# Performance work log

Hardware: AMD Instinct MI355X
Metric: run time of the kernel (lower is better)

Reference implementation:

```python
import jax, jax.numpy as jnp
import numpy as np

D, NH, T = 1024, 16, 2048
DH = D // NH
SCALE = 1.0 / np.sqrt(DH)


def setup_inputs() -> dict:
    key = jax.random.key(0)
    k1, k2, k3, k4 = jax.random.split(key, 4)
    x = jax.random.normal(k1, (4, T, D), dtype=jnp.float32)
    # torch nn.Linear weights: y = x @ W.T ; init scaled like default
    qkv_w = jax.random.normal(k2, (3 * D, D), dtype=jnp.float32) * (1.0 / np.sqrt(D))
    o_w = jax.random.normal(k3, (D, D), dtype=jnp.float32) * (1.0 / np.sqrt(D))
    o_b = jax.random.normal(k4, (D,), dtype=jnp.float32) * 0.01
    return {"x": x, "qkv_w": qkv_w, "o_w": o_w, "o_b": o_b}


def reference(x, qkv_w, o_w, o_b):
    b, t, c = x.shape
    qkv = jnp.einsum('btc,fc->btf', x, qkv_w)  # [b,t,3d]
    q, k, v = jnp.split(qkv, 3, axis=-1)
    # [b, nh, t, dh]
    q = q.reshape(b, t, NH, DH).transpose(0, 2, 1, 3)
    k = k.reshape(b, t, NH, DH).transpose(0, 2, 1, 3)
    v = v.reshape(b, t, NH, DH).transpose(0, 2, 1, 3)
    w = jnp.einsum('bhqd,bhkd->bhqk', q, k) * SCALE
    causal = jnp.tril(jnp.ones((t, t), dtype=bool))
    w = jnp.where(causal[None, None], w, -jnp.inf)
    w = jax.nn.softmax(w, axis=-1)
    out = jnp.einsum('bhqk,bhkd->bhqd', w, v)
    out = out.transpose(0, 2, 1, 3).reshape(b, t, c)
    return jnp.einsum('btc,oc->bto', out, o_w) + o_b
```

## Files before the change

### kernel.cpp

```cpp
#include <hip/hip_runtime.h>
#include <stdint.h>

#define TSEQ   2048
#define SCALE_ATTN 0.125f

typedef __attribute__((ext_vector_type(8))) short bf16x8;
typedef __attribute__((ext_vector_type(4))) short short4v;
typedef __attribute__((ext_vector_type(4))) float f32x4;

__device__ __forceinline__ short f2bf(float f) {
  unsigned u = __float_as_uint(f);
  u = (u + 0x7fffu + ((u >> 16) & 1u)) >> 16;
  return (short)u;
}

__device__ __forceinline__ void async16(const void* gsrc, void* ldst) {
  __builtin_amdgcn_global_load_lds((__attribute__((address_space(1))) void*)(void*)gsrc,
                                   (__attribute__((address_space(3))) void*)ldst, 16, 0, 0);
}

__global__ void cast_f32_bf16(const float* __restrict__ src, short* __restrict__ dst, int n) {
  int i = (blockIdx.x * blockDim.x + threadIdx.x) * 4;
  if (i >= n) return;
  float4 v = *(const float4*)(src + i);
  short4v o;
  o[0] = f2bf(v.x); o[1] = f2bf(v.y); o[2] = f2bf(v.z); o[3] = f2bf(v.w);
  *(short4v*)(dst + i) = o;
}

template<int MODE>
__global__ __launch_bounds__(256, 2) void gemm_bt(
    const short* __restrict__ A, const short* __restrict__ B,
    void* __restrict__ C, short* __restrict__ Cvt, const float* __restrict__ bias,
    int M, int N, int K)
{
  __shared__ char ldsA[128 * 128];
  __shared__ char ldsB[128 * 128];

  const int tid  = threadIdx.x;
  const int lane = tid & 63;
  const int w    = tid >> 6;
  const int wrow = w >> 1, wcol = w & 1;
  const int l15  = lane & 15;
  const int klo  = (lane >> 4) << 4;

  int nwg = gridDim.x, orig = blockIdx.x;
  int qq = nwg >> 3, rr = nwg & 7;
  int xcd = orig & 7, lid = orig >> 3;
  int wgid = (xcd < rr ? xcd * (qq + 1) : rr * (qq + 1) + (xcd - rr) * qq) + lid;
  const int nbx = N >> 7;
  const int by = wgid / nbx, bx = wgid - by * nbx;
  const int m0 = by << 7, n0 = bx << 7;

  const char* Abase = (const char*)A + (size_t)m0 * K * 2;
  const char* Bbase = (const char*)B + (size_t)n0 * K * 2;
  const int rowstride = K * 2;

  const int srow  = tid >> 3;
  const int scolb = (tid & 7) << 4;

  f32x4 acc[4][4] = {};

  const int nk = K >> 6;
  for (int kk = 0; kk < nk; ++kk) {
    if (kk) __syncthreads();
    const int kbyte = kk << 7;
    #pragma unroll
    for (int p = 0; p < 4; ++p) {
      int row = p * 32 + srow;
      int sc  = scolb ^ ((row & 7) << 4);
      async16(Abase + (size_t)row * rowstride + kbyte + sc, ldsA + row * 128 + scolb);
      async16(Bbase + (size_t)row * rowstride + kbyte + sc, ldsB + row * 128 + scolb);
    }
    __syncthreads();

    bf16x8 af[2][4], bf[2][4];
    #pragma unroll
    for (int ks = 0; ks < 2; ++ks)
      #pragma unroll
      for (int mi = 0; mi < 4; ++mi) {
        int row = wrow * 64 + mi * 16 + l15;
        af[ks][mi] = *(const bf16x8*)(ldsA + row * 128 + ((ks * 64 + klo) ^ ((row & 7) << 4)));
      }
    #pragma unroll
    for (int ks = 0; ks < 2; ++ks)
      #pragma unroll
      for (int ni = 0; ni < 4; ++ni) {
        int row = wcol * 64 + ni * 16 + l15;
        bf[ks][ni] = *(const bf16x8*)(ldsB + row * 128 + ((ks * 64 + klo) ^ ((row & 7) << 4)));
      }
    #pragma unroll
    for (int mi = 0; mi < 4; ++mi)
      #pragma unroll
      for (int ni = 0; ni < 4; ++ni) {
        acc[mi][ni] = __builtin_amdgcn_mfma_f32_16x16x32_bf16(af[0][mi], bf[0][ni], acc[mi][ni], 0, 0, 0);
        acc[mi][ni] = __builtin_amdgcn_mfma_f32_16x16x32_bf16(af[1][mi], bf[1][ni], acc[mi][ni], 0, 0, 0);
      }
  }

  const int rbase = (lane >> 4) << 2;
  #pragma unroll
  for (int mi = 0; mi < 4; ++mi)
    #pragma unroll
    for (int ni = 0; ni < 4; ++ni) {
      const int col  = n0 + wcol * 64 + ni * 16 + l15;
      const int row0 = m0 + wrow * 64 + mi * 16 + rbase;
      if (MODE == 0) {
        #pragma unroll
        for (int j = 0; j < 4; ++j)
          ((float*)C)[(size_t)(row0 + j) * N + col] = acc[mi][ni][j] + bias[col];
      } else {
        if (n0 < 2048) {
          #pragma unroll
          for (int j = 0; j < 4; ++j)
            ((short*)C)[(size_t)(row0 + j) * 2048 + col] = f2bf(acc[mi][ni][j]);
        } else {
          short4v o;
          #pragma unroll
          for (int j = 0; j < 4; ++j) o[j] = f2bf(acc[mi][ni][j]);
          const int cv = col - 2048, hh = cv >> 6, dd = cv & 63;
          const int bb = row0 >> 11, t = row0 & 2047;
          *(short4v*)(Cvt + ((size_t)((bb * 16 + hh) * 64 + dd)) * 2048 + t) = o;
        }
      }
    }
}

__global__ __launch_bounds__(64, 2) void attn_wave(
    const short* __restrict__ qk, const short* __restrict__ vt, short* __restrict__ O)
{
  __shared__ short ldsP[32][72];

  const int lane = threadIdx.x;
  const int l15  = lane & 15;
  const int lg   = lane >> 4;

  const int bid = blockIdx.x;
  const int xcd = bid & 7, ii = bid >> 3;
  const int qb  = 63 - (ii >> 3);
  const int bh  = xcd * 8 + (ii & 7);
  const int b   = bh >> 4, h = bh & 15;
  const int q0  = qb * 32;
  const int rowbase = b * TSEQ;

  const short* qbase = qk + (size_t)rowbase * 2048 + h * 64 + lg * 8;
  const short* kbase = qbase + 1024;
  const short* vbase = vt + ((size_t)bh * 64 + l15) * 2048 + lg * 8;

  bf16x8 qf[2][2];
  #pragma unroll
  for (int ks = 0; ks < 2; ++ks)
    #pragma unroll
    for (int mi = 0; mi < 2; ++mi)
      qf[ks][mi] = *(const bf16x8*)(qbase + (size_t)(q0 + mi * 16 + l15) * 2048 + ks * 32);

  f32x4 oacc[2][4] = {};
  float mrun[2][4], lrun[2][4];
  #pragma unroll
  for (int mi = 0; mi < 2; ++mi)
    #pragma unroll
    for (int j = 0; j < 4; ++j) { mrun[mi][j] = -1e30f; lrun[mi][j] = 0.f; }

  const int nst = (qb >> 1) + 1;
  for (int s = 0; s < nst; ++s) {
    const int kv0 = s * 64;

    bf16x8 kf[2][4];
    #pragma unroll
    for (int ks = 0; ks < 2; ++ks)
      #pragma unroll
      for (int ni = 0; ni < 4; ++ni)
        kf[ks][ni] = *(const bf16x8*)(kbase + (size_t)(kv0 + ni * 16 + l15) * 2048 + ks * 32);

    bf16x8 vf[2][4];
    #pragma unroll
    for (int c = 0; c < 2; ++c)
      #pragma unroll
      for (int ni = 0; ni < 4; ++ni)
        vf[c][ni] = *(const bf16x8*)(vbase + (size_t)(ni * 16) * 2048 + kv0 + c * 32);

    f32x4 sacc[2][4] = {};
    #pragma unroll
    for (int mi = 0; mi < 2; ++mi)
      #pragma unroll
      for (int ni = 0; ni < 4; ++ni) {
        sacc[mi][ni] = __builtin_amdgcn_mfma_f32_16x16x32_bf16(qf[0][mi], kf[0][ni], sacc[mi][ni], 0, 0, 0);
        sacc[mi][ni] = __builtin_amdgcn_mfma_f32_16x16x32_bf16(qf[1][mi], kf[1][ni], sacc[mi][ni], 0, 0, 0);
      }

    const bool diag = (s == nst - 1);
    #pragma unroll
    for (int mi = 0; mi < 2; ++mi)
      #pragma unroll
      for (int ni = 0; ni < 4; ++ni)
        #pragma unroll
        for (int j = 0; j < 4; ++j) {
          float sv = sacc[mi][ni][j] * SCALE_ATTN;
          if (diag) {
            int qrow = q0 + mi * 16 + lg * 4 + j;
            int kcol = kv0 + ni * 16 + l15;
            if (kcol > qrow) sv = -1e30f;
          }
          sacc[mi][ni][j] = sv;
        }

    float rmx[2][4];
    #pragma unroll
    for (int mi = 0; mi < 2; ++mi)
      #pragma unroll
      for (int j = 0; j < 4; ++j) {
        float v = fmaxf(fmaxf(sacc[mi][0][j], sacc[mi][1][j]), fmaxf(sacc[mi][2][j], sacc[mi][3][j]));
        v = fmaxf(v, __shfl_xor(v, 1));
        v = fmaxf(v, __shfl_xor(v, 2));
        v = fmaxf(v, __shfl_xor(v, 4));
        v = fmaxf(v, __shfl_xor(v, 8));
        rmx[mi][j] = v;
      }

    #pragma unroll
    for (int mi = 0; mi < 2; ++mi)
      #pragma unroll
      for (int j = 0; j < 4; ++j) {
        float mold = mrun[mi][j];
        float mnew = fmaxf(mold, rmx[mi][j]);
        float alpha = __expf(mold - mnew);
        mrun[mi][j] = mnew;
        float rs = 0.f;
        #pragma unroll
        for (int ni = 0; ni < 4; ++ni) {
          float p = __expf(sacc[mi][ni][j] - mnew);
          rs += p;
          ldsP[mi * 16 + lg * 4 + j][ni * 16 + l15] = f2bf(p);
        }
        rs += __shfl_xor(rs, 1); rs += __shfl_xor(rs, 2);
        rs += __shfl_xor(rs, 4); rs += __shfl_xor(rs, 8);
        lrun[mi][j] = lrun[mi][j] * alpha + rs;
        #pragma unroll
        for (int ni = 0; ni < 4; ++ni) oacc[mi][ni][j] *= alpha;
      }

    asm volatile("" ::: "memory");

    bf16x8 pf[2][2];
    #pragma unroll
    for (int c = 0; c < 2; ++c)
      #pragma unroll
      for (int mi = 0; mi < 2; ++mi)
        pf[c][mi] = *(const bf16x8*)((const char*)&ldsP[mi * 16 + l15][0] + c * 64 + lg * 16);
    #pragma unroll
    for (int mi = 0; mi < 2; ++mi)
      #pragma unroll
      for (int ni = 0; ni < 4; ++ni) {
        oacc[mi][ni] = __builtin_amdgcn_mfma_f32_16x16x32_bf16(pf[0][mi], vf[0][ni], oacc[mi][ni], 0, 0, 0);
        oacc[mi][ni] = __builtin_amdgcn_mfma_f32_16x16x32_bf16(pf[1][mi], vf[1][ni], oacc[mi][ni], 0, 0, 0);
      }
  }

  #pragma unroll
  for (int mi = 0; mi < 2; ++mi)
    #pragma unroll
    for (int ni = 0; ni < 4; ++ni)
      #pragma unroll
      for (int j = 0; j < 4; ++j) {
        int trow = rowbase + q0 + mi * 16 + lg * 4 + j;
        int col  = h * 64 + ni * 16 + l15;
        O[(size_t)trow * 1024 + col] = f2bf(oacc[mi][ni][j] / lrun[mi][j]);
      }
}

extern "C" void kernel_launch(void* const* d_in, const int* in_sizes, int n_in,
                              void* d_out, int out_size, void* d_ws, size_t ws_size,
                              hipStream_t stream) {
  const float* x     = (const float*)d_in[0];
  const float* qkv_w = (const float*)d_in[1];
  const float* o_w   = (const float*)d_in[2];
  const float* o_b   = (const float*)d_in[3];

  char* ws = (char*)d_ws;
  short* xb    = (short*)(ws);
  short* wqkvb = (short*)(ws + 16777216);
  short* wob   = (short*)(ws + 23068672);
  short* qkb   = (short*)(ws + 25165824);
  short* vtb   = (short*)(ws + 58720256);
  short* ob    = (short*)(ws + 75497472);

  cast_f32_bf16<<<8192, 256, 0, stream>>>(x,     xb,    8388608);
  cast_f32_bf16<<<3072, 256, 0, stream>>>(qkv_w, wqkvb, 3145728);
  cast_f32_bf16<<<1024, 256, 0, stream>>>(o_w,   wob,   1048576);

  gemm_bt<2><<<1536, 256, 0, stream>>>(xb, wqkvb, (void*)qkb, vtb, nullptr, 8192, 3072, 1024);

  attn_wave<<<4096, 64, 0, stream>>>(qkb, vtb, ob);

  gemm_bt<0><<<512, 256, 0, stream>>>(ob, wob, d_out, nullptr, o_b, 8192, 1024, 1024);
}
```

Measured before the change: 218.3 us.

## Fold softmax scale into K, use exp2, transpose S tile, pack 4 heads per block

The QKV GEMM epilogue now multiplies K by scale*log2(e), so attention can use the raw exp2 instruction and no longer scales each score. The score tile is computed as K·Qᵀ, which puts each query row in a lane and turns the per-row max and sum reductions into two cross-group shuffles plus in-register reductions, with packed 4-wide LDS stores of P. Four heads for the same query block now run as four waves in one 256-thread block, each with its own LDS slice. The normalisation uses a reciprocal multiply instead of a division. The added cost is shuffles to broadcast alpha and 1/l back into the output layout.

Result: slower. 225.4 us (+3.3%).

```diff
diff --git a/kernel.cpp b/kernel.cpp
--- a/kernel.cpp
+++ b/kernel.cpp
@@ -2,11 +2,13 @@
 #include <stdint.h>
 
 #define TSEQ   2048
-#define SCALE_ATTN 0.125f
+#define SCALE_K 0.18033688011112042f
 
 typedef __attribute__((ext_vector_type(8))) short bf16x8;
 typedef __attribute__((ext_vector_type(4))) short short4v;
 typedef __attribute__((ext_vector_type(4))) float f32x4;
+
+#define EXP2F(x) __builtin_amdgcn_exp2f(x)
 
 __device__ __forceinline__ short f2bf(float f) {
   unsigned u = __float_as_uint(f);
@@ -110,10 +112,14 @@
         for (int j = 0; j < 4; ++j)
           ((float*)C)[(size_t)(row0 + j) * N + col] = acc[mi][ni][j] + bias[col];
       } else {
-        if (n0 < 2048) {
+        if (n0 < 1024) {
           #pragma unroll
           for (int j = 0; j < 4; ++j)
             ((short*)C)[(size_t)(row0 + j) * 2048 + col] = f2bf(acc[mi][ni][j]);
+        } else if (n0 < 2048) {
+          #pragma unroll
+          for (int j = 0; j < 4; ++j)
+            ((short*)C)[(size_t)(row0 + j) * 2048 + col] = f2bf(acc[mi][ni][j] * SCALE_K);
         } else {
           short4v o;
           #pragma unroll
@@ -126,21 +132,23 @@
     }
 }
 
-__global__ __launch_bounds__(64, 2) void attn_wave(
+__global__ __launch_bounds__(256, 3) void attn_wave(
     const short* __restrict__ qk, const short* __restrict__ vt, short* __restrict__ O)
 {
-  __shared__ short ldsP[32][72];
-
-  const int lane = threadIdx.x;
+  __shared__ short ldsP[4][32][72];
+
+  const int tid  = threadIdx.x;
+  const int lane = tid & 63;
+  const int w    = tid >> 6;
   const int l15  = lane & 15;
   const int lg   = lane >> 4;
-
-  const int bid = blockIdx.x;
-  const int xcd = bid & 7, ii = bid >> 3;
-  const int qb  = 63 - (ii >> 3);
-  const int bh  = xcd * 8 + (ii & 7);
-  const int b   = bh >> 4, h = bh & 15;
-  const int q0  = qb * 32;
+  short* ldsPw   = &ldsP[w][0][0];
+
+  const int i  = blockIdx.x;
+  const int qb = 63 - (i >> 4);
+  const int bh = ((i & 15) << 2) + w;
+  const int b  = bh >> 4, h = bh & 15;
+  const int q0 = qb * 32;
   const int rowbase = b * TSEQ;
 
   const short* qbase = qk + (size_t)rowbase * 2048 + h * 64 + lg * 8;
@@ -151,15 +159,11 @@
   #pragma unroll
   for (int ks = 0; ks < 2; ++ks)
     #pragma unroll
-    for (int mi = 0; mi < 2; ++mi)
-      qf[ks][mi] = *(const bf16x8*)(qbase + (size_t)(q0 + mi * 16 + l15) * 2048 + ks * 32);
+    for (int qb2 = 0; qb2 < 2; ++qb2)
+      qf[ks][qb2] = *(const bf16x8*)(qbase + (size_t)(q0 + qb2 * 16 + l15) * 2048 + ks * 32);
 
   f32x4 oacc[2][4] = {};
-  float mrun[2][4], lrun[2][4];
-  #pragma unroll
-  for (int mi = 0; mi < 2; ++mi)
-    #pragma unroll
-    for (int j = 0; j < 4; ++j) { mrun[mi][j] = -1e30f; lrun[mi][j] = 0.f; }
+  float mrun[2] = {-1e30f, -1e30f}, lrun[2] = {0.f, 0.f};
 
   const int nst = (qb >> 1) + 1;
   for (int s = 0; s < nst; ++s) {
@@ -169,9 +173,8 @@
     #pragma unroll
     for (int ks = 0; ks < 2; ++ks)
       #pragma unroll
-      for (int ni = 0; ni < 4; ++ni)
-        kf[ks][ni] = *(const bf16x8*)(kbase + (size_t)(kv0 + ni * 16 + l15) * 2048 + ks * 32);
-
+      for (int kb = 0; kb < 4; ++kb)
+        kf[ks][kb] = *(const bf16x8*)(kbase + (size_t)(kv0 + kb * 16 + l15) * 2048 + ks * 32);
     bf16x8 vf[2][4];
     #pragma unroll
     for (int c = 0; c < 2; ++c)
@@ -179,64 +182,65 @@
       for (int ni = 0; ni < 4; ++ni)
         vf[c][ni] = *(const bf16x8*)(vbase + (size_t)(ni * 16) * 2048 + kv0 + c * 32);
 
-    f32x4 sacc[2][4] = {};
+    f32x4 sacc[4][2] = {};
+    #pragma unroll
+    for (int kb = 0; kb < 4; ++kb)
+      #pragma unroll
+      for (int qb2 = 0; qb2 < 2; ++qb2) {
+        sacc[kb][qb2] = __builtin_amdgcn_mfma_f32_16x16x32_bf16(kf[0][kb], qf[0][qb2], sacc[kb][qb2], 0, 0, 0);
+        sacc[kb][qb2] = __builtin_amdgcn_mfma_f32_16x16x32_bf16(kf[1][kb], qf[1][qb2], sacc[kb][qb2], 0, 0, 0);
+      }
+
+    if (s == nst - 1) {
+      #pragma unroll
+      for (int kb = 0; kb < 4; ++kb)
+        #pragma unroll
+        for (int qb2 = 0; qb2 < 2; ++qb2) {
+          int qrow = q0 + qb2 * 16 + l15;
+          #pragma unroll
+          for (int j = 0; j < 4; ++j)
+            if (kv0 + kb * 16 + lg * 4 + j > qrow) sacc[kb][qb2][j] = -1e30f;
+        }
+    }
+
+    float alpha[2];
+    #pragma unroll
+    for (int qb2 = 0; qb2 < 2; ++qb2) {
+      float t0 = fmaxf(fmaxf(sacc[0][qb2][0], sacc[0][qb2][1]), fmaxf(sacc[0][qb2][2], sacc[0][qb2][3]));
+      float t1 = fmaxf(fmaxf(sacc[1][qb2][0], sacc[1][qb2][1]), fmaxf(sacc[1][qb2][2], sacc[1][qb2][3]));
+      float t2 = fmaxf(fmaxf(sacc[2][qb2][0], sacc[2][qb2][1]), fmaxf(sacc[2][qb2][2], sacc[2][qb2][3]));
+      float t3 = fmaxf(fmaxf(sacc[3][qb2][0], sacc[3][qb2][1]), fmaxf(sacc[3][qb2][2], sacc[3][qb2][3]));
+      float v  = fmaxf(fmaxf(t0, t1), fmaxf(t2, t3));
+      v = fmaxf(v, __shfl_xor(v, 16));
+      v = fmaxf(v, __shfl_xor(v, 32));
+      float mold = mrun[qb2];
+      float mnew = fmaxf(mold, v);
+      alpha[qb2] = EXP2F(mold - mnew);
+      mrun[qb2]  = mnew;
+      float rs = 0.f;
+      #pragma unroll
+      for (int kb = 0; kb < 4; ++kb) {
+        float p0 = EXP2F(sacc[kb][qb2][0] - mnew);
+        float p1 = EXP2F(sacc[kb][qb2][1] - mnew);
+        float p2 = EXP2F(sacc[kb][qb2][2] - mnew);
+        float p3 = EXP2F(sacc[kb][qb2][3] - mnew);
+        rs += (p0 + p1) + (p2 + p3);
+        short4v ps;
+        ps[0] = f2bf(p0); ps[1] = f2bf(p1); ps[2] = f2bf(p2); ps[3] = f2bf(p3);
+        *(short4v*)((char*)ldsPw + (qb2 * 16 + l15) * 144 + kb * 32 + lg * 8) = ps;
+      }
+      rs += __shfl_xor(rs, 16);
+      rs += __shfl_xor(rs, 32);
+      lrun[qb2] = lrun[qb2] * alpha[qb2] + rs;
+    }
+
     #pragma unroll
     for (int mi = 0; mi < 2; ++mi)
       #pragma unroll
-      for (int ni = 0; ni < 4; ++ni) {
-        sacc[mi][ni] = __builtin_amdgcn_mfma_f32_16x16x32_bf16(qf[0][mi], kf[0][ni], sacc[mi][ni], 0, 0, 0);
-        sacc[mi][ni] = __builtin_amdgcn_mfma_f32_16x16x32_bf16(qf[1][mi], kf[1][ni], sacc[mi][ni], 0, 0, 0);
-      }
-
-    const bool diag = (s == nst - 1);
-    #pragma unroll
-    for (int mi = 0; mi < 2; ++mi)
-      #pragma unroll
-      for (int ni = 0; ni < 4; ++ni)
+      for (int j = 0; j < 4; ++j) {
+        float ar = __shfl(alpha[mi], lg * 4 + j);
         #pragma unroll
-        for (int j = 0; j < 4; ++j) {
-          float sv = sacc[mi][ni][j] * SCALE_ATTN;
-          if (diag) {
-            int qrow = q0 + mi * 16 + lg * 4 + j;
-            int kcol = kv0 + ni * 16 + l15;
-            if (kcol > qrow) sv = -1e30f;
-          }
-          sacc[mi][ni][j] = sv;
-        }
-
-    float rmx[2][4];
-    #pragma unroll
-    for (int mi = 0; mi < 2; ++mi)
-      #pragma unroll
-      for (int j = 0; j < 4; ++j) {
-        float v = fmaxf(fmaxf(sacc[mi][0][j], sacc[mi][1][j]), fmaxf(sacc[mi][2][j], sacc[mi][3][j]));
-        v = fmaxf(v, __shfl_xor(v, 1));
-        v = fmaxf(v, __shfl_xor(v, 2));
-        v = fmaxf(v, __shfl_xor(v, 4));
-        v = fmaxf(v, __shfl_xor(v, 8));
-        rmx[mi][j] = v;
-      }
-
-    #pragma unroll
-    for (int mi = 0; mi < 2; ++mi)
-      #pragma unroll
-      for (int j = 0; j < 4; ++j) {
-        float mold = mrun[mi][j];
-        float mnew = fmaxf(mold, rmx[mi][j]);
-        float alpha = __expf(mold - mnew);
-        mrun[mi][j] = mnew;
-        float rs = 0.f;
-        #pragma unroll
-        for (int ni = 0; ni < 4; ++ni) {
-          float p = __expf(sacc[mi][ni][j] - mnew);
-          rs += p;
-          ldsP[mi * 16 + lg * 4 + j][ni * 16 + l15] = f2bf(p);
-        }
-        rs += __shfl_xor(rs, 1); rs += __shfl_xor(rs, 2);
-        rs += __shfl_xor(rs, 4); rs += __shfl_xor(rs, 8);
-        lrun[mi][j] = lrun[mi][j] * alpha + rs;
-        #pragma unroll
-        for (int ni = 0; ni < 4; ++ni) oacc[mi][ni][j] *= alpha;
+        for (int ni = 0; ni < 4; ++ni) oacc[mi][ni][j] *= ar;
       }
 
     asm volatile("" ::: "memory");
@@ -246,7 +250,10 @@
     for (int c = 0; c < 2; ++c)
       #pragma unroll
       for (int mi = 0; mi < 2; ++mi)
-        pf[c][mi] = *(const bf16x8*)((const char*)&ldsP[mi * 16 + l15][0] + c * 64 + lg * 16);
+        pf[c][mi] = *(const bf16x8*)((const char*)ldsPw + (mi * 16 + l15) * 144 + c * 64 + lg * 16);
+
+    asm volatile("" ::: "memory");
+
     #pragma unroll
     for (int mi = 0; mi < 2; ++mi)
       #pragma unroll
@@ -257,15 +264,19 @@
   }
 
   #pragma unroll
-  for (int mi = 0; mi < 2; ++mi)
-    #pragma unroll
-    for (int ni = 0; ni < 4; ++ni)
-      #pragma unroll
-      for (int j = 0; j < 4; ++j) {
-        int trow = rowbase + q0 + mi * 16 + lg * 4 + j;
-        int col  = h * 64 + ni * 16 + l15;
-        O[(size_t)trow * 1024 + col] = f2bf(oacc[mi][ni][j] / lrun[mi][j]);
-      }
+  for (int mi = 0; mi < 2; ++mi) {
+    float linv = 1.0f / lrun[mi];
+    #pragma unroll
+    for (int j = 0; j < 4; ++j) {
+      float lr = __shfl(linv, lg * 4 + j);
+      int trow = rowbase + q0 + mi * 16 + lg * 4 + j;
+      #pragma unroll
+      for (int ni = 0; ni < 4; ++ni) {
+        int col = h * 64 + ni * 16 + l15;
+        O[(size_t)trow * 1024 + col] = f2bf(oacc[mi][ni][j] * lr);
+      }
+    }
+  }
 }
 
 extern "C" void kernel_launch(void* const* d_in, const int* in_sizes, int n_in,
@@ -290,7 +301,7 @@
 
   gemm_bt<2><<<1536, 256, 0, stream>>>(xb, wqkvb, (void*)qkb, vtb, nullptr, 8192, 3072, 1024);
 
-  attn_wave<<<4096, 64, 0, stream>>>(qkb, vtb, ob);
+  attn_wave<<<1024, 256, 0, stream>>>(qkb, vtb, ob);
 
   gemm_bt<0><<<512, 256, 0, stream>>>(ob, wob, d_out, nullptr, o_b, 8192, 1024, 1024);
 }
```
